# Kernel optimization log

Measured on AMD Instinct MI355X. Metric: run time of the kernel, lower is better.

The kernel has to match this reference:

```python
import jax, jax.numpy as jnp
import numpy as np

N_NODES = 50000
N_EDGES = 400000
IN_DIM = 64
HID = 128
HEADS = 4
NEG_SLOPE = 0.2


def gat_conv(x, src, dst, W, a_src, a_dst, b, heads, out_ch, concat):
    N = x.shape[0]
    h = (x @ W).reshape(N, heads, out_ch)                 # [N,H,C]
    alpha_s = jnp.einsum('nhc,hc->nh', h, a_src)          # [N,H]
    alpha_d = jnp.einsum('nhc,hc->nh', h, a_dst)
    e = jax.nn.leaky_relu(alpha_s[src] + alpha_d[dst], NEG_SLOPE)  # [E,H]
    m = jax.ops.segment_max(e, dst, num_segments=N)
    m = jnp.where(jnp.isfinite(m), m, 0.0)
    ex = jnp.exp(e - m[dst])
    s = jax.ops.segment_sum(ex, dst, num_segments=N)
    alpha = ex / s[dst]                                   # segment softmax over incoming edges
    out = jax.ops.segment_sum(h[src] * alpha[:, :, None], dst, num_segments=N)  # [N,H,C]
    out = out.reshape(N, heads * out_ch) if concat else out.mean(axis=1)
    return out + b


def setup_inputs() -> dict:
    key = jax.random.key(0)
    ks = jax.random.split(key, 20)
    g = lambda i, shape, sc: (jax.random.normal(ks[i], shape, jnp.float32) * sc)
    x = g(0, (N_NODES, IN_DIM), 1.0)
    edge_index = jax.random.randint(ks[1], (2, N_EDGES), 0, N_NODES, dtype=jnp.int32)
    d = {
        'x': x, 'edge_index': edge_index,
        'W1': g(2, (IN_DIM, HEADS * HID), 0.1), 'a_src1': g(3, (HEADS, HID), 0.1), 'a_dst1': g(4, (HEADS, HID), 0.1), 'b1': jnp.zeros((HEADS * HID,), jnp.float32),
        'W2': g(5, (HEADS * HID, HEADS * HID), 0.05), 'a_src2': g(6, (HEADS, HID), 0.1), 'a_dst2': g(7, (HEADS, HID), 0.1), 'b2': jnp.zeros((HEADS * HID,), jnp.float32),
        'W3': g(8, (HEADS * HID, HID), 0.05), 'a_src3': g(9, (1, HID), 0.1), 'a_dst3': g(10, (1, HID), 0.1), 'b3': jnp.zeros((HID,), jnp.float32),
        'fc1_w': g(11, (HID, HID // 2), 0.1), 'fc1_b': jnp.zeros((HID // 2,), jnp.float32),
        'fc2_w': g(12, (HID // 2, 1), 0.1), 'fc2_b': jnp.zeros((1,), jnp.float32),
    }
    return d


def reference(x, edge_index, W1, a_src1, a_dst1, b1, W2, a_src2, a_dst2, b2, W3, a_src3, a_dst3, b3, fc1_w, fc1_b, fc2_w, fc2_b):
    N = x.shape[0]
    loop = jnp.arange(N, dtype=edge_index.dtype)
    src = jnp.concatenate([edge_index[0], loop])  # PyG GATConv adds self-loops by default
    dst = jnp.concatenate([edge_index[1], loop])
    h = jax.nn.elu(gat_conv(x, src, dst, W1, a_src1, a_dst1, b1, HEADS, HID, True))
    h = jax.nn.elu(gat_conv(h, src, dst, W2, a_src2, a_dst2, b2, HEADS, HID, True))
    h = jax.nn.elu(gat_conv(h, src, dst, W3, a_src3, a_dst3, b3, 1, HID, False))
    h = jax.nn.relu(h @ fc1_w + fc1_b)
    return jax.nn.sigmoid(h @ fc2_w + fc2_b)  # [N, 1]
```

## Files before the change

### kernel.cpp

```cpp
#include <hip/hip_runtime.h>
#include <math.h>

typedef __attribute__((ext_vector_type(8))) short short8;
typedef __attribute__((ext_vector_type(4))) float f32x4;
typedef unsigned short u16;
typedef unsigned int u32;

__device__ inline u16 f2b(float f) {
  u32 u = __float_as_uint(f);
  return (u16)((u + 0x7FFFu + ((u >> 16) & 1u)) >> 16);
}
__device__ inline float b2f(u16 b) { return __uint_as_float((u32)b << 16); }
__device__ inline float lrelu(float v) { return v > 0.f ? v : 0.2f * v; }

__device__ inline void gld_lds16(const void* g, void* l) {
  __builtin_amdgcn_global_load_lds((const __attribute__((address_space(1))) void*)g,
                                   (__attribute__((address_space(3))) void*)l, 16, 0, 0);
}

__global__ void fused_prep(const float* __restrict__ x, u16* __restrict__ xb, int NX,
                           const float* __restrict__ W1, u16* __restrict__ Wt1,
                           const float* __restrict__ W2, u16* __restrict__ Wt2,
                           const float* __restrict__ W3, u16* __restrict__ Wt3,
                           const int* __restrict__ ei, int E0, int ET,
                           int* __restrict__ deg) {
  int i = blockIdx.x * blockDim.x + threadIdx.x;
  if (i < NX) {
    xb[i] = f2b(x[i]);
    return;
  }
  i -= NX;
  if (i < 64 * 512) {
    int k = i / 512, n = i % 512;
    Wt1[n * 64 + k] = f2b(W1[i]);
    return;
  }
  i -= 64 * 512;
  if (i < 512 * 512) {
    int k = i / 512, n = i % 512;
    Wt2[n * 512 + k] = f2b(W2[i]);
    return;
  }
  i -= 512 * 512;
  if (i < 512 * 128) {
    int k = i / 128, n = i % 128;
    Wt3[n * 512 + k] = f2b(W3[i]);
    return;
  }
  i -= 512 * 128;
  if (i < ET) {
    int d = (i < E0) ? ei[E0 + i] : (i - E0);
    atomicAdd(&deg[d], 1);
  }
}

__global__ __launch_bounds__(256) void gemm_bf16_gat(
    const u16* __restrict__ A, const u16* __restrict__ Bt, u16* __restrict__ Hb,
    const float* __restrict__ a_src, const float* __restrict__ a_dst,
    float* __restrict__ aS, float* __restrict__ aD, int M, int HC, int K, int Hh) {
  __shared__ u16 As[128 * 32];
  __shared__ u16 Bs[128 * 32];
  __shared__ float sRed[2][2][128];
  const int tid = threadIdx.x;
  const int w = tid >> 6, lane = tid & 63;
  const int wm = w >> 1, wn = w & 1;
  const int q = lane >> 4, l15 = lane & 15;
  const int nBase = blockIdx.x * 128;
  const int mBase = blockIdx.y * 128;
  const int h = nBase >> 7;
  const int srow = lane >> 2;
  const int skc = (lane & 3) * 8;

  f32x4 acc[4][4];
#pragma unroll
  for (int i = 0; i < 4; ++i)
#pragma unroll
    for (int j = 0; j < 4; ++j) acc[i][j] = (f32x4){0.f, 0.f, 0.f, 0.f};

  for (int k0 = 0; k0 < K; k0 += 32) {
#pragma unroll
    for (int r = 0; r < 2; ++r) {
      int lrow = w * 32 + r * 16 + srow;
      int ga = mBase + lrow;
      if (ga >= M) ga = M - 1;
      gld_lds16(A + (size_t)ga * K + k0 + skc, &As[(w * 32 + r * 16) * 32]);
      int gb = nBase + lrow;
      gld_lds16(Bt + (size_t)gb * K + k0 + skc, &Bs[(w * 32 + r * 16) * 32]);
    }
    __syncthreads();
    short8 af[4], bf[4];
#pragma unroll
    for (int i = 0; i < 4; ++i)
      af[i] = *(const short8*)&As[(wm * 64 + i * 16 + l15) * 32 + q * 8];
#pragma unroll
    for (int j = 0; j < 4; ++j)
      bf[j] = *(const short8*)&Bs[(wn * 64 + j * 16 + l15) * 32 + q * 8];
#pragma unroll
    for (int i = 0; i < 4; ++i)
#pragma unroll
      for (int j = 0; j < 4; ++j)
        acc[i][j] = __builtin_amdgcn_mfma_f32_16x16x32_bf16(af[i], bf[j], acc[i][j], 0, 0, 0);
    __syncthreads();
  }

  float asv[4], adv[4];
#pragma unroll
  for (int j = 0; j < 4; ++j) {
    int cw = wn * 64 + j * 16 + l15;
    asv[j] = a_src[h * 128 + cw];
    adv[j] = a_dst[h * 128 + cw];
  }
#pragma unroll
  for (int mi = 0; mi < 4; ++mi) {
#pragma unroll
    for (int r = 0; r < 4; ++r) {
      int row = mBase + wm * 64 + mi * 16 + q * 4 + r;
      float s = 0.f, d = 0.f;
#pragma unroll
      for (int j = 0; j < 4; ++j) {
        float v = acc[mi][j][r];
        s = fmaf(v, asv[j], s);
        d = fmaf(v, adv[j], d);
        if (row < M) Hb[(size_t)row * HC + nBase + wn * 64 + j * 16 + l15] = f2b(v);
      }
#pragma unroll
      for (int o = 8; o; o >>= 1) {
        s += __shfl_xor(s, o);
        d += __shfl_xor(d, o);
      }
      if (l15 == 0) {
        int lr = wm * 64 + mi * 16 + q * 4 + r;
        sRed[0][wn][lr] = s;
        sRed[1][wn][lr] = d;
      }
    }
  }
  __syncthreads();
  if (tid < 128) {
    int row = mBase + tid;
    if (row < M) {
      aS[(size_t)row * Hh + h] = sRed[0][0][tid] + sRed[0][1][tid];
      aD[(size_t)row * Hh + h] = sRed[1][0][tid] + sRed[1][1][tid];
    }
  }
}

__global__ __launch_bounds__(256) void scan_chunk(const int* __restrict__ deg,
                                                  int* __restrict__ incl,
                                                  int* __restrict__ bsums, int N) {
  __shared__ int sdata[256];
  const int t = threadIdx.x;
  const int base = blockIdx.x * 2048;
  int v[8];
  int sum = 0;
#pragma unroll
  for (int i = 0; i < 8; ++i) {
    int idx = base + t * 8 + i;
    v[i] = (idx < N) ? deg[idx] : 0;
    sum += v[i];
  }
  sdata[t] = sum;
  __syncthreads();
  for (int off = 1; off < 256; off <<= 1) {
    int x = (t >= off) ? sdata[t - off] : 0;
    __syncthreads();
    sdata[t] += x;
    __syncthreads();
  }
  int run = (t > 0) ? sdata[t - 1] : 0;
#pragma unroll
  for (int i = 0; i < 8; ++i) {
    int idx = base + t * 8 + i;
    run += v[i];
    if (idx < N) incl[idx] = run;
  }
  if (t == 255) bsums[blockIdx.x] = sdata[255];
}

__global__ void scan_final(const int* __restrict__ incl, const int* __restrict__ bsums,
                           int* __restrict__ rowptr, int N, int nb) {
  int i = blockIdx.x * blockDim.x + threadIdx.x;
  if (i >= N) return;
  int chunk = i >> 11;
  int pre = 0;
  for (int j = 0; j < chunk; ++j) pre += bsums[j];
  rowptr[i + 1] = incl[i] + pre;
  if (i == 0) rowptr[0] = 0;
}

__global__ void csr_fill(const int* __restrict__ ei, int E0, int ET,
                         const int* __restrict__ rowptr, int* __restrict__ cnt,
                         int* __restrict__ csr_src) {
  int e = blockIdx.x * blockDim.x + threadIdx.x;
  if (e >= ET) return;
  int s, d;
  if (e < E0) { s = ei[e]; d = ei[E0 + e]; }
  else        { s = e - E0; d = e - E0; }
  int pos = atomicAdd(&cnt[d], 1);
  csr_src[rowptr[d] + pos] = s;
}

#define ACC8(pv, wgt)                                             \
  acc[0] = fmaf(wgt, b2f((u16)(pv.x & 0xffff)), acc[0]);          \
  acc[1] = fmaf(wgt, b2f((u16)(pv.x >> 16)), acc[1]);             \
  acc[2] = fmaf(wgt, b2f((u16)(pv.y & 0xffff)), acc[2]);          \
  acc[3] = fmaf(wgt, b2f((u16)(pv.y >> 16)), acc[3]);             \
  acc[4] = fmaf(wgt, b2f((u16)(pv.z & 0xffff)), acc[4]);          \
  acc[5] = fmaf(wgt, b2f((u16)(pv.z >> 16)), acc[5]);             \
  acc[6] = fmaf(wgt, b2f((u16)(pv.w & 0xffff)), acc[6]);          \
  acc[7] = fmaf(wgt, b2f((u16)(pv.w >> 16)), acc[7]);

__global__ __launch_bounds__(256) void gat_fused_agg(
    const int* __restrict__ rowptr, const int* __restrict__ csr_src,
    const u16* __restrict__ Hb, const float* __restrict__ aSb,
    const float* __restrict__ aDb, const float* __restrict__ bias,
    u16* __restrict__ outB, float* __restrict__ outF, int N) {
  const int wid = (int)((blockIdx.x * (blockDim.x >> 6)) + (threadIdx.x >> 6));
  const int lane = threadIdx.x & 63;
  if (wid >= N) return;
  const int beg = rowptr[wid];
  const int deg = rowptr[wid + 1] - beg;

  const int h = lane >> 4;
  const int e16 = lane & 15;
  const int c0 = lane * 8;
  const int hbase = lane & 48;
  const float adh = aDb[(size_t)wid * 4 + h];
  float bv[8];
  *(float4*)&bv[0] = *(const float4*)&bias[c0];
  *(float4*)&bv[4] = *(const float4*)&bias[c0 + 4];
  float m = -1e30f, ssum = 0.f;
  float acc[8] = {};
  for (int c = 0; c < deg; c += 16) {
    const int ce = min(16, deg - c);
    int srcv = 0;
    float l = -1e30f;
    if (e16 < ce) {
      srcv = csr_src[beg + c + e16];
      l = lrelu(aSb[(size_t)srcv * 4 + h] + adh);
    }
    float cm = l;
#pragma unroll
    for (int o = 8; o; o >>= 1) cm = fmaxf(cm, __shfl_xor(cm, o));
    float pexp, cs;
    if (c == 0) {
      m = cm;
      pexp = expf(l - m);
      cs = pexp;
#pragma unroll
      for (int o = 8; o; o >>= 1) cs += __shfl_xor(cs, o);
      ssum = cs;
    } else {
      float newm = fmaxf(m, cm);
      float r = expf(m - newm);
      m = newm;
      pexp = expf(l - m);
      cs = pexp;
#pragma unroll
      for (int o = 8; o; o >>= 1) cs += __shfl_xor(cs, o);
      ssum = ssum * r + cs;
#pragma unroll
      for (int i = 0; i < 8; ++i) acc[i] *= r;
    }
    int e = 0;
    for (; e + 4 <= ce; e += 4) {
      int se0 = __shfl(srcv, e + 0), se1 = __shfl(srcv, e + 1);
      int se2 = __shfl(srcv, e + 2), se3 = __shfl(srcv, e + 3);
      float w0 = __shfl(pexp, hbase | (e + 0)), w1 = __shfl(pexp, hbase | (e + 1));
      float w2 = __shfl(pexp, hbase | (e + 2)), w3 = __shfl(pexp, hbase | (e + 3));
      uint4 p0 = *(const uint4*)&Hb[(size_t)se0 * 512 + c0];
      uint4 p1 = *(const uint4*)&Hb[(size_t)se1 * 512 + c0];
      uint4 p2 = *(const uint4*)&Hb[(size_t)se2 * 512 + c0];
      uint4 p3 = *(const uint4*)&Hb[(size_t)se3 * 512 + c0];
      ACC8(p0, w0)
      ACC8(p1, w1)
      ACC8(p2, w2)
      ACC8(p3, w3)
    }
    for (; e < ce; ++e) {
      int se = __shfl(srcv, e);
      float wgt = __shfl(pexp, hbase | e);
      uint4 pv = *(const uint4*)&Hb[(size_t)se * 512 + c0];
      ACC8(pv, wgt)
    }
  }
  const float inv = 1.f / ssum;
  u16 packed[8];
#pragma unroll
  for (int i = 0; i < 8; ++i) {
    float v = fmaf(acc[i], inv, bv[i]);
    v = v > 0.f ? v : expm1f(v);
    acc[i] = v;
    packed[i] = f2b(v);
  }
  if (outB) *(uint4*)&outB[(size_t)wid * 512 + c0] = *(const uint4*)packed;
  if (outF) {
    *(float4*)&outF[(size_t)wid * 512 + c0] = make_float4(acc[0], acc[1], acc[2], acc[3]);
    *(float4*)&outF[(size_t)wid * 512 + c0 + 4] =
        make_float4(acc[4], acc[5], acc[6], acc[7]);
  }
}

__global__ __launch_bounds__(256) void gat_agg_h1(
    const int* __restrict__ rowptr, const int* __restrict__ csr_src,
    const u16* __restrict__ Hb, const float* __restrict__ aSb,
    const float* __restrict__ aDb, const float* __restrict__ bias,
    float* __restrict__ outF, int N) {
  const int wid = (int)((blockIdx.x * (blockDim.x >> 6)) + (threadIdx.x >> 6));
  const int lane = threadIdx.x & 63;
  if (wid >= N) return;
  const int beg = rowptr[wid];
  const int deg = rowptr[wid + 1] - beg;
  const int g = lane & 15;
  const int es = lane >> 4;
  const int c0 = g * 8;
  const float adh = aDb[wid];
  float m = -1e30f, ssum = 0.f;
  float acc[8] = {};
  for (int c = 0; c < deg; c += 64) {
    const int ce = min(64, deg - c);
    int srcv = 0;
    float l = -1e30f;
    if (lane < ce) {
      srcv = csr_src[beg + c + lane];
      l = lrelu(aSb[srcv] + adh);
    }
    float cm = l;
#pragma unroll
    for (int o = 32; o; o >>= 1) cm = fmaxf(cm, __shfl_xor(cm, o));
    float pexp, cs;
    if (c == 0) {
      m = cm;
      pexp = expf(l - m);
      cs = pexp;
#pragma unroll
      for (int o = 32; o; o >>= 1) cs += __shfl_xor(cs, o);
      ssum = cs;
    } else {
      float newm = fmaxf(m, cm);
      float r = expf(m - newm);
      m = newm;
      pexp = expf(l - m);
      cs = pexp;
#pragma unroll
      for (int o = 32; o; o >>= 1) cs += __shfl_xor(cs, o);
      ssum = ssum * r + cs;
#pragma unroll
      for (int i = 0; i < 8; ++i) acc[i] *= r;
    }
    for (int t = 0; t < ce; t += 4) {
      int idx = t + es;
      int se = __shfl(srcv, idx & 63);
      float wgt = __shfl(pexp, idx & 63);
      if (idx < ce) {
        uint4 pv = *(const uint4*)&Hb[(size_t)se * 128 + c0];
        ACC8(pv, wgt)
      }
    }
  }
#pragma unroll
  for (int i = 0; i < 8; ++i) {
    acc[i] += __shfl_xor(acc[i], 16);
    acc[i] += __shfl_xor(acc[i], 32);
  }
  if (lane < 16) {
    const float inv = 1.f / ssum;
    float o[8];
#pragma unroll
    for (int i = 0; i < 8; ++i) {
      float v = fmaf(acc[i], inv, bias[c0 + i]);
      o[i] = v > 0.f ? v : expm1f(v);
    }
    *(float4*)&outF[(size_t)wid * 128 + c0] = make_float4(o[0], o[1], o[2], o[3]);
    *(float4*)&outF[(size_t)wid * 128 + c0 + 4] = make_float4(o[4], o[5], o[6], o[7]);
  }
}

__global__ __launch_bounds__(256) void fc_head(const float* __restrict__ A,
                                               const float* __restrict__ B,
                                               const float* __restrict__ bias,
                                               const float* __restrict__ w2,
                                               const float* __restrict__ b2,
                                               float* __restrict__ out, int M) {
  __shared__ float As[16][64];
  __shared__ float Bs[16][64];
  __shared__ float sP[64][17];
  const int tid = threadIdx.x;
  const int tx = tid & 15, ty = tid >> 4;
  const int mBase = blockIdx.y * 64;
  const int aRow = tid >> 2;
  const int aK = (tid & 3) << 2;
  const int bC = tid & 63;
  const int bR0 = tid >> 6;
  const int K = 128, N = 64;
  float acc[4][4] = {};
  for (int k0 = 0; k0 < K; k0 += 16) {
    float4 av = make_float4(0.f, 0.f, 0.f, 0.f);
    int gr = mBase + aRow;
    if (gr < M) av = *(const float4*)&A[(size_t)gr * K + k0 + aK];
    As[aK + 0][aRow] = av.x;
    As[aK + 1][aRow] = av.y;
    As[aK + 2][aRow] = av.z;
    As[aK + 3][aRow] = av.w;
#pragma unroll
    for (int i = 0; i < 4; ++i) {
      int r = bR0 + i * 4;
      Bs[r][bC] = B[(size_t)(k0 + r) * N + bC];
    }
    __syncthreads();
#pragma unroll
    for (int k = 0; k < 16; ++k) {
      float4 a = *(const float4*)&As[k][ty * 4];
      float4 b = *(const float4*)&Bs[k][tx * 4];
      float ar[4] = {a.x, a.y, a.z, a.w};
      float br[4] = {b.x, b.y, b.z, b.w};
#pragma unroll
      for (int i = 0; i < 4; ++i)
#pragma unroll
        for (int j = 0; j < 4; ++j) acc[i][j] = fmaf(ar[i], br[j], acc[i][j]);
    }
    __syncthreads();
  }
  float4 bv = *(const float4*)&bias[tx * 4];
  float4 wv = *(const float4*)&w2[tx * 4];
#pragma unroll
  for (int i = 0; i < 4; ++i) {
    float p = 0.f;
    p = fmaf(fmaxf(acc[i][0] + bv.x, 0.f), wv.x, p);
    p = fmaf(fmaxf(acc[i][1] + bv.y, 0.f), wv.y, p);
    p = fmaf(fmaxf(acc[i][2] + bv.z, 0.f), wv.z, p);
    p = fmaf(fmaxf(acc[i][3] + bv.w, 0.f), wv.w, p);
    sP[ty * 4 + i][tx] = p;
  }
  __syncthreads();
  if (tid < 64) {
    int row = mBase + tid;
    if (row < M) {
      float s = 0.f;
#pragma unroll
      for (int t = 0; t < 16; ++t) s += sP[tid][t];
      out[row] = 1.f / (1.f + expf(-(s + b2[0])));
    }
  }
}

extern "C" void kernel_launch(void* const* d_in, const int* in_sizes, int n_in,
                              void* d_out, int out_size, void* d_ws, size_t ws_size,
                              hipStream_t stream) {
  const float* x    = (const float*)d_in[0];
  const int*   ei   = (const int*)d_in[1];
  const float* W1   = (const float*)d_in[2];
  const float* as1  = (const float*)d_in[3];
  const float* ad1  = (const float*)d_in[4];
  const float* b1   = (const float*)d_in[5];
  const float* W2   = (const float*)d_in[6];
  const float* as2  = (const float*)d_in[7];
  const float* ad2  = (const float*)d_in[8];
  const float* b2   = (const float*)d_in[9];
  const float* W3   = (const float*)d_in[10];
  const float* as3  = (const float*)d_in[11];
  const float* ad3  = (const float*)d_in[12];
  const float* b3   = (const float*)d_in[13];
  const float* fc1w = (const float*)d_in[14];
  const float* fc1b = (const float*)d_in[15];
  const float* fc2w = (const float*)d_in[16];
  const float* fc2b = (const float*)d_in[17];
  float* out = (float*)d_out;

  const int N  = in_sizes[0] / 64;
  const int E0 = in_sizes[1] / 2;
  const int ET = E0 + N;

  char* ws = (char*)d_ws;
  size_t off = 0;
  auto alloc = [&](size_t bytes) -> void* {
    void* p = ws + off;
    off += (bytes + 255) & ~(size_t)255;
    return p;
  };
  u16*   bufXb   = (u16*)alloc((size_t)N * 512 * 2);
  u16*   bufHb   = (u16*)alloc((size_t)N * 512 * 2);
  float* bufF    = (float*)alloc((size_t)N * 128 * 4);
  float* aS      = (float*)alloc((size_t)N * 4 * 4);
  float* aD      = (float*)alloc((size_t)N * 4 * 4);
  u16*   Wt1     = (u16*)alloc((size_t)512 * 64 * 2);
  u16*   Wt2     = (u16*)alloc((size_t)512 * 512 * 2);
  u16*   Wt3     = (u16*)alloc((size_t)128 * 512 * 2);
  int*   degcnt  = (int*)alloc((size_t)2 * N * 4);
  int*   deg     = degcnt;
  int*   cnt     = degcnt + N;
  int*   incl    = (int*)alloc((size_t)N * 4);
  int*   rowptr  = (int*)alloc((size_t)(N + 1) * 4);
  int*   bsums   = (int*)alloc(256 * 4);
  int*   csr_src = (int*)alloc((size_t)ET * 4);
  (void)ws_size; (void)n_in; (void)out_size;

  hipMemsetAsync(degcnt, 0, (size_t)2 * N * 4, stream);
  const int NX = N * 64;
  const int prepTotal = NX + 64 * 512 + 512 * 512 + 512 * 128 + ET;
  hipLaunchKernelGGL(fused_prep, dim3((prepTotal + 255) / 256), dim3(256), 0, stream, x,
                     bufXb, NX, W1, Wt1, W2, Wt2, W3, Wt3, ei, E0, ET, deg);

  int nb = (N + 2047) / 2048;
  hipLaunchKernelGGL(scan_chunk, dim3(nb), dim3(256), 0, stream, deg, incl, bsums, N);
  hipLaunchKernelGGL(scan_final, dim3((N + 255) / 256), dim3(256), 0, stream, incl, bsums,
                     rowptr, N, nb);
  int eb = (ET + 255) / 256;
  hipLaunchKernelGGL(csr_fill, dim3(eb), dim3(256), 0, stream, ei, E0, ET, rowptr, cnt,
                     csr_src);

  const int gy = (N + 127) / 128;

  hipLaunchKernelGGL(gemm_bf16_gat, dim3(4, gy), dim3(256), 0, stream, bufXb, Wt1, bufHb,
                     as1, ad1, aS, aD, N, 512, 64, 4);
  hipLaunchKernelGGL(gat_fused_agg, dim3((N + 3) / 4), dim3(256), 0, stream, rowptr,
                     csr_src, bufHb, aS, aD, b1, bufXb, nullptr, N);
  hipLaunchKernelGGL(gemm_bf16_gat, dim3(4, gy), dim3(256), 0, stream, bufXb, Wt2, bufHb,
                     as2, ad2, aS, aD, N, 512, 512, 4);
  hipLaunchKernelGGL(gat_fused_agg, dim3((N + 3) / 4), dim3(256), 0, stream, rowptr,
                     csr_src, bufHb, aS, aD, b2, bufXb, nullptr, N);
  hipLaunchKernelGGL(gemm_bf16_gat, dim3(1, gy), dim3(256), 0, stream, bufXb, Wt3, bufHb,
                     as3, ad3, aS, aD, N, 128, 512, 1);
  hipLaunchKernelGGL(gat_agg_h1, dim3((N + 3) / 4), dim3(256), 0, stream, rowptr, csr_src,
                     bufHb, aS, aD, b3, bufF, N);

  hipLaunchKernelGGL(fc_head, dim3(1, (N + 63) / 64), dim3(256), 0, stream, bufF, fc1w,
                     fc1b, fc2w, fc2b, out, N);
}
```

Before: 464.5 us.

## Fuse CSR construction into one cooperative kernel and swizzle GEMM blocks across XCDs

```diff
diff --git a/kernel.cpp b/kernel.cpp
--- a/kernel.cpp
+++ b/kernel.cpp
@@ -1,5 +1,8 @@
 #include <hip/hip_runtime.h>
+#include <hip/hip_cooperative_groups.h>
 #include <math.h>
+
+namespace cg = cooperative_groups;
 
 typedef __attribute__((ext_vector_type(8))) short short8;
 typedef __attribute__((ext_vector_type(4))) float f32x4;
@@ -21,9 +24,7 @@
 __global__ void fused_prep(const float* __restrict__ x, u16* __restrict__ xb, int NX,
                            const float* __restrict__ W1, u16* __restrict__ Wt1,
                            const float* __restrict__ W2, u16* __restrict__ Wt2,
-                           const float* __restrict__ W3, u16* __restrict__ Wt3,
-                           const int* __restrict__ ei, int E0, int ET,
-                           int* __restrict__ deg) {
+                           const float* __restrict__ W3, u16* __restrict__ Wt3) {
   int i = blockIdx.x * blockDim.x + threadIdx.x;
   if (i < NX) {
     xb[i] = f2b(x[i]);
@@ -45,19 +46,103 @@
   if (i < 512 * 128) {
     int k = i / 128, n = i % 128;
     Wt3[n * 512 + k] = f2b(W3[i]);
-    return;
-  }
-  i -= 512 * 128;
-  if (i < ET) {
-    int d = (i < E0) ? ei[E0 + i] : (i - E0);
+  }
+}
+
+__global__ __launch_bounds__(256) void csr_build_coop(
+    const int* __restrict__ ei, int E0, int ET, int N, int* __restrict__ degcnt,
+    int* __restrict__ incl, int* __restrict__ bsums, int* __restrict__ rowptr,
+    int* __restrict__ csr_src) {
+  cg::grid_group grid = cg::this_grid();
+  __shared__ int sdata[256];
+  int* deg = degcnt;
+  int* cnt = degcnt + N;
+  const int t = threadIdx.x;
+  const int gsize = gridDim.x * blockDim.x;
+  const int gtid = blockIdx.x * blockDim.x + t;
+  const int nb = (N + 2047) / 2048;
+
+  for (int i = gtid; i < 2 * N; i += gsize) degcnt[i] = 0;
+  grid.sync();
+
+  for (int e = gtid; e < ET; e += gsize) {
+    int d = (e < E0) ? ei[E0 + e] : (e - E0);
     atomicAdd(&deg[d], 1);
+  }
+  grid.sync();
+
+  for (int b = blockIdx.x; b < nb; b += gridDim.x) {
+    const int base = b * 2048;
+    int v[8];
+    int sum = 0;
+#pragma unroll
+    for (int i = 0; i < 8; ++i) {
+      int idx = base + t * 8 + i;
+      v[i] = (idx < N) ? deg[idx] : 0;
+      sum += v[i];
+    }
+    sdata[t] = sum;
+    __syncthreads();
+    for (int off = 1; off < 256; off <<= 1) {
+      int x = (t >= off) ? sdata[t - off] : 0;
+      __syncthreads();
+      sdata[t] += x;
+      __syncthreads();
+    }
+    int run = (t > 0) ? sdata[t - 1] : 0;
+#pragma unroll
+    for (int i = 0; i < 8; ++i) {
+      int idx = base + t * 8 + i;
+      run += v[i];
+      if (idx < N) incl[idx] = run;
+    }
+    if (t == 255) bsums[b] = sdata[255];
+    __syncthreads();
+  }
+  grid.sync();
+
+  if (blockIdx.x == 0) {
+    sdata[t] = (t < nb) ? bsums[t] : 0;
+    __syncthreads();
+    for (int off = 1; off < 256; off <<= 1) {
+      int x = (t >= off) ? sdata[t - off] : 0;
+      __syncthreads();
+      sdata[t] += x;
+      __syncthreads();
+    }
+    if (t < nb) bsums[t] = (t == 0) ? 0 : sdata[t - 1];
+  }
+  grid.sync();
+
+  for (int i = gtid; i < N; i += gsize) rowptr[i + 1] = incl[i] + bsums[i >> 11];
+  if (gtid == 0) rowptr[0] = 0;
+  grid.sync();
+
+  for (int e = gtid; e < ET; e += gsize) {
+    int s, d;
+    if (e < E0) { s = ei[e]; d = ei[E0 + e]; }
+    else        { s = e - E0; d = e - E0; }
+    int pos = atomicAdd(&cnt[d], 1);
+    csr_src[rowptr[d] + pos] = s;
   }
 }
 
 __global__ __launch_bounds__(256) void gemm_bf16_gat(
     const u16* __restrict__ A, const u16* __restrict__ Bt, u16* __restrict__ Hb,
     const float* __restrict__ a_src, const float* __restrict__ a_dst,
-    float* __restrict__ aS, float* __restrict__ aD, int M, int HC, int K, int Hh) {
+    float* __restrict__ aS, float* __restrict__ aD, int M, int HC, int K, int Hh,
+    int gy, int nStrips) {
+  int mIdx, nIdx;
+  if (nStrips == 4) {
+    int l = blockIdx.x;
+    int xcd = l & 7, k = l >> 3;
+    nIdx = k & 3;
+    mIdx = xcd + 8 * (k >> 2);
+    if (mIdx >= gy) return;
+  } else {
+    mIdx = blockIdx.x;
+    nIdx = 0;
+  }
   __shared__ u16 As[128 * 32];
   __shared__ u16 Bs[128 * 32];
   __shared__ float sRed[2][2][128];
@@ -65,8 +150,8 @@
   const int w = tid >> 6, lane = tid & 63;
   const int wm = w >> 1, wn = w & 1;
   const int q = lane >> 4, l15 = lane & 15;
-  const int nBase = blockIdx.x * 128;
-  const int mBase = blockIdx.y * 128;
+  const int nBase = nIdx * 128;
+  const int mBase = mIdx * 128;
   const int h = nBase >> 7;
   const int srow = lane >> 2;
   const int skc = (lane & 3) * 8;
@@ -143,61 +228,6 @@
       aD[(size_t)row * Hh + h] = sRed[1][0][tid] + sRed[1][1][tid];
     }
   }
-}
-
-__global__ __launch_bounds__(256) void scan_chunk(const int* __restrict__ deg,
-                                                  int* __restrict__ incl,
-                                                  int* __restrict__ bsums, int N) {
-  __shared__ int sdata[256];
-  const int t = threadIdx.x;
-  const int base = blockIdx.x * 2048;
-  int v[8];
-  int sum = 0;
-#pragma unroll
-  for (int i = 0; i < 8; ++i) {
-    int idx = base + t * 8 + i;
-    v[i] = (idx < N) ? deg[idx] : 0;
-    sum += v[i];
-  }
-  sdata[t] = sum;
-  __syncthreads();
-  for (int off = 1; off < 256; off <<= 1) {
-    int x = (t >= off) ? sdata[t - off] : 0;
-    __syncthreads();
-    sdata[t] += x;
-    __syncthreads();
-  }
-  int run = (t > 0) ? sdata[t - 1] : 0;
-#pragma unroll
-  for (int i = 0; i < 8; ++i) {
-    int idx = base + t * 8 + i;
-    run += v[i];
-    if (idx < N) incl[idx] = run;
-  }
-  if (t == 255) bsums[blockIdx.x] = sdata[255];
-}
-
-__global__ void scan_final(const int* __restrict__ incl, const int* __restrict__ bsums,
-                           int* __restrict__ rowptr, int N, int nb) {
-  int i = blockIdx.x * blockDim.x + threadIdx.x;
-  if (i >= N) return;
-  int chunk = i >> 11;
-  int pre = 0;
-  for (int j = 0; j < chunk; ++j) pre += bsums[j];
-  rowptr[i + 1] = incl[i] + pre;
-  if (i == 0) rowptr[0] = 0;
-}
-
-__global__ void csr_fill(const int* __restrict__ ei, int E0, int ET,
-                         const int* __restrict__ rowptr, int* __restrict__ cnt,
-                         int* __restrict__ csr_src) {
-  int e = blockIdx.x * blockDim.x + threadIdx.x;
-  if (e >= ET) return;
-  int s, d;
-  if (e < E0) { s = ei[e]; d = ei[E0 + e]; }
-  else        { s = e - E0; d = e - E0; }
-  int pos = atomicAdd(&cnt[d], 1);
-  csr_src[rowptr[d] + pos] = s;
 }
 
 #define ACC8(pv, wgt)                                             \
@@ -487,40 +517,45 @@
   u16*   Wt2     = (u16*)alloc((size_t)512 * 512 * 2);
   u16*   Wt3     = (u16*)alloc((size_t)128 * 512 * 2);
   int*   degcnt  = (int*)alloc((size_t)2 * N * 4);
-  int*   deg     = degcnt;
-  int*   cnt     = degcnt + N;
   int*   incl    = (int*)alloc((size_t)N * 4);
   int*   rowptr  = (int*)alloc((size_t)(N + 1) * 4);
   int*   bsums   = (int*)alloc(256 * 4);
   int*   csr_src = (int*)alloc((size_t)ET * 4);
   (void)ws_size; (void)n_in; (void)out_size;
 
-  hipMemsetAsync(degcnt, 0, (size_t)2 * N * 4, stream);
   const int NX = N * 64;
-  const int prepTotal = NX + 64 * 512 + 512 * 512 + 512 * 128 + ET;
+  const int prepTotal = NX + 64 * 512 + 512 * 512 + 512 * 128;
   hipLaunchKernelGGL(fused_prep, dim3((prepTotal + 255) / 256), dim3(256), 0, stream, x,
-                     bufXb, NX, W1, Wt1, W2, Wt2, W3, Wt3, ei, E0, ET, deg);
-
-  int nb = (N + 2047) / 2048;
-  hipLaunchKernelGGL(scan_chunk, dim3(nb), dim3(256), 0, stream, deg, incl, bsums, N);
-  hipLaunchKernelGGL(scan_final, dim3((N + 255) / 256), dim3(256), 0, stream, incl, bsums,
-                     rowptr, N, nb);
-  int eb = (ET + 255) / 256;
-  hipLaunchKernelGGL(csr_fill, dim3(eb), dim3(256), 0, stream, ei, E0, ET, rowptr, cnt,
-                     csr_src);
+                     bufXb, NX, W1, Wt1, W2, Wt2, W3, Wt3);
+
+  {
+    const int* ei_a = ei;
+    int E0_a = E0, ET_a = ET, N_a = N;
+    int* degcnt_a = degcnt;
+    int* incl_a = incl;
+    int* bsums_a = bsums;
+    int* rowptr_a = rowptr;
+    int* csr_a = csr_src;
+    void* args[] = {(void*)&ei_a, (void*)&E0_a, (void*)&ET_a, (void*)&N_a,
+                    (void*)&degcnt_a, (void*)&incl_a, (void*)&bsums_a,
+                    (void*)&rowptr_a, (void*)&csr_a};
+    hipLaunchCooperativeKernel((void*)csr_build_coop, dim3(1024), dim3(256), args, 0,
+                               stream);
+  }
 
   const int gy = (N + 127) / 128;
-
-  hipLaunchKernelGGL(gemm_bf16_gat, dim3(4, gy), dim3(256), 0, stream, bufXb, Wt1, bufHb,
-                     as1, ad1, aS, aD, N, 512, 64, 4);
+  const int grid4 = ((gy + 7) / 8) * 8 * 4;
+
+  hipLaunchKernelGGL(gemm_bf16_gat, dim3(grid4), dim3(256), 0, stream, bufXb, Wt1, bufHb,
+                     as1, ad1, aS, aD, N, 512, 64, 4, gy, 4);
   hipLaunchKernelGGL(gat_fused_agg, dim3((N + 3) / 4), dim3(256), 0, stream, rowptr,
                      csr_src, bufHb, aS, aD, b1, bufXb, nullptr, N);
-  hipLaunchKernelGGL(gemm_bf16_gat, dim3(4, gy), dim3(256), 0, stream, bufXb, Wt2, bufHb,
-                     as2, ad2, aS, aD, N, 512, 512, 4);
+  hipLaunchKernelGGL(gemm_bf16_gat, dim3(grid4), dim3(256), 0, stream, bufXb, Wt2, bufHb,
+                     as2, ad2, aS, aD, N, 512, 512, 4, gy, 4);
   hipLaunchKernelGGL(gat_fused_agg, dim3((N + 3) / 4), dim3(256), 0, stream, rowptr,
                      csr_src, bufHb, aS, aD, b2, bufXb, nullptr, N);
-  hipLaunchKernelGGL(gemm_bf16_gat, dim3(1, gy), dim3(256), 0, stream, bufXb, Wt3, bufHb,
-                     as3, ad3, aS, aD, N, 128, 512, 1);
+  hipLaunchKernelGGL(gemm_bf16_gat, dim3(gy), dim3(256), 0, stream, bufXb, Wt3, bufHb,
+                     as3, ad3, aS, aD, N, 128, 512, 1, gy, 1);
   hipLaunchKernelGGL(gat_agg_h1, dim3((N + 3) / 4), dim3(256), 0, stream, rowptr, csr_src,
                      bufHb, aS, aD, b3, bufF, N);
 
```

After: 933.9 us. +101.0%, slower.
